# Optimization experiments

Hardware: AMD Instinct MI355X
Metric: run time of the kernel (lower is better)

The kernel has to match this reference:

```python
import jax, jax.numpy as jnp
import numpy as np

B, T, DIM, N_EMBED = 16, 2048, 512, 4096


def setup_inputs() -> dict:
    key = jax.random.key(0)
    k1, k2 = jax.random.split(key)
    x = jax.random.normal(k1, (B, T, DIM), dtype=jnp.float32)
    embed_weight = jax.random.normal(k2, (N_EMBED, DIM), dtype=jnp.float32)
    return {"x": x, "embed_weight": embed_weight}


def reference(x, embed_weight):
    dim = embed_weight.shape[1]
    # embed = embedding.weight.detach().T, column-normalized -> [dim, n_embed]
    w = jax.lax.stop_gradient(embed_weight).T
    w = w / jnp.linalg.norm(w, axis=0, keepdims=True)
    flatten = jax.lax.stop_gradient(x).reshape(-1, dim)  # [N, dim]
    # squared-distance expansion: |f|^2 - 2 f.w + |w|^2 -> [N, n_embed]
    dist = (
        jnp.sum(flatten * flatten, axis=1, keepdims=True)
        - 2.0 * (flatten @ w)
        + jnp.sum(w * w, axis=0, keepdims=True)
    )
    embed_ind = jnp.argmax(-dist, axis=1).reshape(x.shape[:-1])  # [B, T]
    # gather from the UN-normalized embedding table (as in the torch code)
    quantize = embed_weight[embed_ind]  # [B, T, dim]
    diff = jnp.mean(jnp.square(quantize - x))
    quantize_1 = x + jax.lax.stop_gradient(quantize - x)  # straight-through
    return ((quantize + quantize_1) * 0.5, diff)
```

## Files before the change

kernel.cpp:

```cpp
#include <hip/hip_runtime.h>
#include <math.h>

#define N_TOK   32768
#define N_CODE  4096
#define DIM     512

#define CBM 64
#define NHALF 2048
#define CBN 256
#define CBK 64
#define NT_STEPS (NHALF / CBN)
#define KC_STEPS (DIM / CBK)
#define SPITCH 36
#define BUFSZ 40960

#define SFENCE() __builtin_amdgcn_sched_barrier(0)

#define BARL() do { \
    SFENCE(); \
    asm volatile("s_waitcnt lgkmcnt(0)" ::: "memory"); \
    __builtin_amdgcn_s_barrier(); \
    SFENCE(); \
} while (0)

#define BAR_PUB10() do { \
    SFENCE(); \
    asm volatile("s_waitcnt vmcnt(10)" ::: "memory"); \
    __builtin_amdgcn_s_barrier(); \
    SFENCE(); \
} while (0)

#define BAR_PUB0() do { \
    SFENCE(); \
    asm volatile("s_waitcnt vmcnt(0)" ::: "memory"); \
    __builtin_amdgcn_s_barrier(); \
    SFENCE(); \
} while (0)

typedef __bf16 bf16x8 __attribute__((ext_vector_type(8)));
typedef float  f32x4  __attribute__((ext_vector_type(4)));

__device__ __forceinline__ unsigned short f32_to_bf16_rn(float f) {
    union { float f; unsigned int u; } c; c.f = f;
    unsigned int u = c.u;
    return (unsigned short)((u + 0x7FFFu + ((u >> 16) & 1u)) >> 16);
}

__device__ __forceinline__ unsigned f32_sortkey(float f) {
    unsigned u = __float_as_uint(f);
    return u ^ ((unsigned)(((int)u) >> 31) | 0x80000000u);
}

__device__ __forceinline__ void top8k_insert(unsigned s, unsigned (&bv)[8]) {
#pragma unroll
    for (int k = 7; k > 0; --k) {
        unsigned t = bv[k] > s ? bv[k] : s;
        bv[k] = (s > bv[k - 1]) ? bv[k - 1] : t;
    }
    bv[0] = bv[0] > s ? bv[0] : s;
}

__device__ __forceinline__ void top3k_insert(unsigned s, unsigned &b0,
                                             unsigned &b1, unsigned &b2) {
    unsigned t = b0 < s ? b0 : s;
    b0 = b0 > s ? b0 : s;
    unsigned u = b1 < t ? b1 : t;
    b1 = b1 > t ? b1 : t;
    b2 = b2 > u ? b2 : u;
}

__device__ __forceinline__ float pairwise_tree(const float* p) {
    float P[4];
#pragma unroll
    for (int b = 0; b < 4; ++b) {
        float t01 = __fadd_rn(p[b * 8 + 0], p[b * 8 + 1]);
        float t23 = __fadd_rn(p[b * 8 + 2], p[b * 8 + 3]);
        float t45 = __fadd_rn(p[b * 8 + 4], p[b * 8 + 5]);
        float t67 = __fadd_rn(p[b * 8 + 6], p[b * 8 + 7]);
        P[b] = __fadd_rn(__fadd_rn(t01, t23), __fadd_rn(t45, t67));
    }
    return __fadd_rn(__fadd_rn(P[0], P[1]), __fadd_rn(P[2], P[3]));
}

__global__ void norms_kernel(const float* __restrict__ embed,
                             float* __restrict__ n_f,
                             float* __restrict__ t3_f) {
    __shared__ float part[32];
    int j = blockIdx.x;
    int lane = threadIdx.x;
    const float* e = embed + (size_t)j * DIM;

    if (lane < 32) {
        int base = (lane >> 3) * 128 + (lane & 7);
        float v = e[base];
        float r = __fmul_rn(v, v);
#pragma unroll
        for (int i = 1; i < 16; ++i) {
            float u = e[base + 8 * i];
            r = __fadd_rn(r, __fmul_rn(u, u));
        }
        part[lane] = r;
    }
    __syncthreads();
    float S = pairwise_tree(part);
    float n = __fsqrt_rn(S);
    __syncthreads();

    if (lane < 32) {
        int base = (lane >> 3) * 128 + (lane & 7);
        float w0 = __fdiv_rn(e[base], n);
        float r = __fmul_rn(w0, w0);
#pragma unroll
        for (int i = 1; i < 16; ++i) {
            float w = __fdiv_rn(e[base + 8 * i], n);
            r = __fadd_rn(r, __fmul_rn(w, w));
        }
        part[lane] = r;
    }
    __syncthreads();
    if (lane == 0) {
        n_f[j]  = n;
        t3_f[j] = pairwise_tree(part);
    }
}

__global__ void xcvt_kernel(const float* __restrict__ x, unsigned short* __restrict__ xb) {
    int gid = blockIdx.x * 256 + threadIdx.x;
    float4 v = ((const float4*)x)[gid];
    ushort4 o;
    o.x = f32_to_bf16_rn(v.x); o.y = f32_to_bf16_rn(v.y);
    o.z = f32_to_bf16_rn(v.z); o.w = f32_to_bf16_rn(v.w);
    ((ushort4*)xb)[gid] = o;
}

__global__ void wcvt_kernel(const float* __restrict__ embed, const float* __restrict__ n_f,
                            float* __restrict__ whf, unsigned short* __restrict__ wb) {
    int gid = blockIdx.x * 256 + threadIdx.x;
    int row = gid >> 7;
    float n = n_f[row];
    float4 e = ((const float4*)embed)[gid];
    float4 w;
    w.x = __fdiv_rn(e.x, n); w.y = __fdiv_rn(e.y, n);
    w.z = __fdiv_rn(e.z, n); w.w = __fdiv_rn(e.w, n);
    ((float4*)whf)[gid] = w;
    ushort4 o;
    o.x = f32_to_bf16_rn(w.x); o.y = f32_to_bf16_rn(w.y);
    o.z = f32_to_bf16_rn(w.z); o.w = f32_to_bf16_rn(w.w);
    ((ushort4*)wb)[gid] = o;
}

__global__ __launch_bounds__(256, 2) void coarse_kernel(
        const unsigned short* __restrict__ xb,
        const unsigned short* __restrict__ wb,
        unsigned* __restrict__ candp) {
    __shared__ __attribute__((aligned(16))) char smem[2 * BUFSZ];

    const int tid  = threadIdx.x;
    const int w    = tid >> 6;
    const int l    = tid & 63;
    const int m0   = (blockIdx.x >> 1) * CBM;
    const int half = blockIdx.x & 1;
    const int n0   = half * NHALF;

    const int srow   = l >> 3;
    const int schunk = (l & 7) ^ srow;
    const int mrow   = l & 15;
    const int kq     = l >> 4;
    const int sw     = mrow & 7;

    const int aoff0 = mrow * 128 + (kq        ^ sw) * 16;
    const int aoff1 = mrow * 128 + ((kq ^ 4)  ^ sw) * 16;
    const int boff0 = 8192 + w * 8192 + mrow * 128 + (kq       ^ sw) * 16;
    const int boff1 = 8192 + w * 8192 + mrow * 128 + ((kq ^ 4) ^ sw) * 16;

    const unsigned short* gA0 = xb + (size_t)(m0 + w * 16 +     srow) * DIM + schunk * 8;
    const unsigned short* gA1 = xb + (size_t)(m0 + w * 16 + 8 + srow) * DIM + schunk * 8;
    const unsigned short* gB[8];
#pragma unroll
    for (int c = 0; c < 8; ++c)
        gB[c] = wb + (size_t)(n0 + w * 64 + c * 8 + srow) * DIM + schunk * 8;

    const int dA = w * 2048;
    const int dB = 8192 + w * 8192;

    auto STAGE = [&](int dstbuf, int koff) {
        char* db = smem + dstbuf * BUFSZ;
        __builtin_amdgcn_global_load_lds(
            (const __attribute__((address_space(1))) void*)(gA0 + koff),
            (__attribute__((address_space(3))) void*)(db + dA), 16, 0, 0);
        __builtin_amdgcn_global_load_lds(
            (const __attribute__((address_space(1))) void*)(gA1 + koff),
            (__attribute__((address_space(3))) void*)(db + dA + 1024), 16, 0, 0);
#pragma unroll
        for (int c = 0; c < 8; ++c)
            __builtin_amdgcn_global_load_lds(
                (const __attribute__((address_space(1))) void*)(gB[c] + koff),
                (__attribute__((address_space(3))) void*)(db + dB + c * 1024), 16, 0, 0);
    };

    unsigned* const sS  = (unsigned*)(smem + BUFSZ);
    unsigned* const swp = sS + w * (64 * SPITCH) + kq * (4 * SPITCH) + mrow;
    const uint4* const srp = (const uint4*)(sS + (tid >> 6) * (64 * SPITCH) + (tid & 63) * SPITCH);

    const int invb = 4095 - n0 - w * 64 - mrow;

    unsigned b0 = 0u, b1 = 0u, b2 = 0u;

    STAGE(0, 0);

    for (int nt = 0; nt < NT_STEPS; ++nt) {
        f32x4 acc[4][4];
#pragma unroll
        for (int i = 0; i < 4; ++i)
#pragma unroll
            for (int j = 0; j < 4; ++j) acc[i][j] = {0.0f, 0.0f, 0.0f, 0.0f};

#pragma unroll
        for (int kc = 0; kc < KC_STEPS; ++kc) {
            if (kc > 0) BARL();

            if (kc < KC_STEPS - 1) {
                STAGE((kc + 1) & 1, (kc + 1) * CBK);
                BAR_PUB10();
            } else if (nt < NT_STEPS - 1) {
#pragma unroll
                for (int c = 0; c < 8; ++c) gB[c] += (size_t)CBN * DIM;
                STAGE(0, 0);
                BAR_PUB10();
            } else {
                BAR_PUB0();
            }

            const int bb = (kc & 1) * BUFSZ;
            bf16x8 a0[4], bb0[4], a1[4], bb1[4];
#pragma unroll
            for (int i = 0; i < 4; ++i)
                a0[i] = *(const bf16x8*)(smem + bb + aoff0 + i * 2048);
#pragma unroll
            for (int j = 0; j < 4; ++j)
                bb0[j] = *(const bf16x8*)(smem + bb + boff0 + j * 2048);
#pragma unroll
            for (int i = 0; i < 4; ++i)
#pragma unroll
                for (int j = 0; j < 4; ++j)
                    acc[i][j] = __builtin_amdgcn_mfma_f32_16x16x32_bf16(
                        a0[i], bb0[j], acc[i][j], 0, 0, 0);
#pragma unroll
            for (int i = 0; i < 4; ++i)
                a1[i] = *(const bf16x8*)(smem + bb + aoff1 + i * 2048);
#pragma unroll
            for (int j = 0; j < 4; ++j)
                bb1[j] = *(const bf16x8*)(smem + bb + boff1 + j * 2048);
#pragma unroll
            for (int i = 0; i < 4; ++i)
#pragma unroll
                for (int j = 0; j < 4; ++j)
                    acc[i][j] = __builtin_amdgcn_mfma_f32_16x16x32_bf16(
                        a1[i], bb1[j], acc[i][j], 0, 0, 0);
        }

        BARL();
#pragma unroll
        for (int h = 0; h < 2; ++h) {
#pragma unroll
            for (int i = 0; i < 4; ++i)
#pragma unroll
                for (int jj = 0; jj < 2; ++jj) {
                    const int j = h * 2 + jj;
                    const unsigned ifld = (unsigned)(invb - (nt * 256 + h * 32 + jj * 16));
#pragma unroll
                    for (int r = 0; r < 4; ++r) {
                        unsigned key = (f32_sortkey(acc[i][j][r]) & 0xFFFFF000u) | ifld;
                        swp[(i * 16 + r) * SPITCH + jj * 16] = key;
                    }
                }
            BARL();
#pragma unroll
            for (int c4 = 0; c4 < 8; ++c4) {
                uint4 v = srp[c4];
                top3k_insert(v.x, b0, b1, b2);
                top3k_insert(v.y, b0, b1, b2);
                top3k_insert(v.z, b0, b1, b2);
                top3k_insert(v.w, b0, b1, b2);
            }
            BARL();
        }
    }

    {
        int tok = tid & 63, qq = tid >> 6;
        unsigned* cp = candp + ((size_t)(m0 + tok) * 2 + half) * 12 + qq * 3;
        cp[0] = b0; cp[1] = b1; cp[2] = b2;
    }
}

__global__ void merge_kernel(const unsigned* __restrict__ candp, int* __restrict__ cand8) {
    int tok = blockIdx.x * 256 + threadIdx.x;
    unsigned bv[8];
#pragma unroll
    for (int k = 0; k < 8; ++k) bv[k] = 0u;
    const unsigned* cp = candp + (size_t)tok * 24;
#pragma unroll
    for (int t = 0; t < 24; ++t) top8k_insert(cp[t], bv);
    int* o = cand8 + (size_t)tok * 8;
#pragma unroll
    for (int k = 0; k < 8; ++k) o[k] = 4095 - (int)(bv[k] & 0xFFFu);
}

__global__ void refine_kernel(const float* __restrict__ x,
                              const float* __restrict__ embed,
                              const float* __restrict__ whf,
                              const float* __restrict__ t3_f,
                              const int* __restrict__ cand,
                              float* __restrict__ out,
                              double* __restrict__ partial) {
    __shared__ float part[4][32];
    __shared__ double wsum[4];
    const int wid  = threadIdx.x >> 6;
    const int lane = threadIdx.x & 63;
    const int tok  = blockIdx.x * 4 + wid;
    const float* f = x + (size_t)tok * DIM;

    if (lane < 32) {
        int base = (lane >> 3) * 128 + (lane & 7);
        float v = f[base];
        float r = __fmul_rn(v, v);
#pragma unroll
        for (int i = 1; i < 16; ++i) {
            float u = f[base + 8 * i];
            r = __fadd_rn(r, __fmul_rn(u, u));
        }
        part[wid][lane] = r;
    }
    __syncthreads();
    float t1 = pairwise_tree(part[wid]);

    float4 f0 = *(const float4*)(f + lane * 8);
    float4 f1 = *(const float4*)(f + lane * 8 + 4);

    float bd = 1e30f; int bc = 0x7fffffff;
    const int* cp = cand + (size_t)tok * 8;
#pragma unroll
    for (int k = 0; k < 8; ++k) {
        int c = cp[k];
        const float* wh = whf + (size_t)c * DIM + lane * 8;
        float4 w0 = *(const float4*)wh;
        float4 w1 = *(const float4*)(wh + 4);
        double s = (double)f0.x * w0.x + (double)f0.y * w0.y
                 + (double)f0.z * w0.z + (double)f0.w * w0.w
                 + (double)f1.x * w1.x + (double)f1.y * w1.y
                 + (double)f1.z * w1.z + (double)f1.w * w1.w;
#pragma unroll
        for (int off = 32; off > 0; off >>= 1) s += __shfl_xor(s, off);
        float mm = (float)s;
        float dist = __fadd_rn(__fsub_rn(t1, __fmul_rn(2.0f, mm)), t3_f[c]);
        if (dist < bd || (dist == bd && c < bc)) { bd = dist; bc = c; }
    }

    const float* eb = embed + (size_t)bc * DIM;
    double dsum = 0.0;
#pragma unroll
    for (int r = 0; r < DIM / 64; ++r) {
        int d = lane + 64 * r;
        float q = eb[d];
        out[(size_t)tok * DIM + d] = q;
        double dd = (double)q - (double)f[d];
        dsum += dd * dd;
    }
#pragma unroll
    for (int off = 32; off > 0; off >>= 1) dsum += __shfl_xor(dsum, off);
    if (lane == 0) wsum[wid] = dsum;
    __syncthreads();
    if (threadIdx.x == 0)
        partial[blockIdx.x] = wsum[0] + wsum[1] + wsum[2] + wsum[3];
}

__global__ void finalize_kernel(const double* __restrict__ partial,
                                float* __restrict__ out) {
    __shared__ double acc[4];
    int tid = threadIdx.x;
    double s = 0.0;
    for (int i = tid; i < N_TOK / 4; i += 256) s += partial[i];
#pragma unroll
    for (int off = 32; off > 0; off >>= 1) s += __shfl_xor(s, off);
    if ((tid & 63) == 0) acc[tid >> 6] = s;
    __syncthreads();
    if (tid == 0)
        out[(size_t)N_TOK * DIM] =
            (float)((acc[0] + acc[1] + acc[2] + acc[3]) * (1.0 / ((double)N_TOK * DIM)));
}

extern "C" void kernel_launch(void* const* d_in, const int* in_sizes, int n_in,
                              void* d_out, int out_size, void* d_ws, size_t ws_size,
                              hipStream_t stream) {
    const float* x     = (const float*)d_in[0];
    const float* embed = (const float*)d_in[1];
    float* out = (float*)d_out;

    char* wsb = (char*)d_ws;
    size_t off = 0;
    double* partial = (double*)(wsb + off); off += 65536;
    float*  n_f     = (float*) (wsb + off); off += 16384;
    float*  t3_f    = (float*) (wsb + off); off += 16384;
    unsigned* candp = (unsigned*)(wsb + off); off += (size_t)N_TOK * 24 * 4;
    int*    cand8   = (int*)   (wsb + off); off += (size_t)N_TOK * 8 * 4;
    unsigned short* xb = (unsigned short*)(wsb + off); off += (size_t)N_TOK * DIM * 2;
    unsigned short* wb = (unsigned short*)(wsb + off); off += (size_t)N_CODE * DIM * 2;
    float*  whf     = (float*) (wsb + off);

    xcvt_kernel    <<<16384, 256, 0, stream>>>(x, xb);
    norms_kernel   <<<N_CODE, 64, 0, stream>>>(embed, n_f, t3_f);
    wcvt_kernel    <<<2048, 256, 0, stream>>>(embed, n_f, whf, wb);
    coarse_kernel  <<<(N_TOK / CBM) * 2, 256, 0, stream>>>(xb, wb, candp);
    merge_kernel   <<<N_TOK / 256, 256, 0, stream>>>(candp, cand8);
    refine_kernel  <<<N_TOK / 4, 256, 0, stream>>>(x, embed, whf, t3_f, cand8, out, partial);
    finalize_kernel<<<1, 256, 0, stream>>>(partial, out);
}
```

Baseline: 373.5 us.

## Keep per-token top-3 candidates in registers and reduce in-block before writing

Swaps the MFMA operand order so each lane's accumulator rows map to a single token. The per-tile LDS transpose plus its two barriers go away, and top-3 tracking runs directly in registers with one list per accumulator row. At the end, the 16 per-lane top-3 lists for each token are merged through LDS into a top-8, which shrinks the candidate buffer and the merge work. The register pressure of 12 extra keys and the more serial insert chain per lane may affect occupancy. Candidate recall also changes, since each token's list now comes from per-lane top-3 over a different column split.

```diff
diff --git a/kernel.cpp b/kernel.cpp
--- a/kernel.cpp
+++ b/kernel.cpp
@@ -11,7 +11,6 @@
 #define CBK 64
 #define NT_STEPS (NHALF / CBN)
 #define KC_STEPS (DIM / CBK)
-#define SPITCH 36
 #define BUFSZ 40960
 
 #define SFENCE() __builtin_amdgcn_sched_barrier(0)
@@ -198,13 +197,9 @@
                 (__attribute__((address_space(3))) void*)(db + dB + c * 1024), 16, 0, 0);
     };
 
-    unsigned* const sS  = (unsigned*)(smem + BUFSZ);
-    unsigned* const swp = sS + w * (64 * SPITCH) + kq * (4 * SPITCH) + mrow;
-    const uint4* const srp = (const uint4*)(sS + (tid >> 6) * (64 * SPITCH) + (tid & 63) * SPITCH);
-
-    const int invb = 4095 - n0 - w * 64 - mrow;
-
-    unsigned b0 = 0u, b1 = 0u, b2 = 0u;
+    unsigned k0[4], k1[4], k2[4];
+#pragma unroll
+    for (int i = 0; i < 4; ++i) { k0[i] = 0u; k1[i] = 0u; k2[i] = 0u; }
 
     STAGE(0, 0);
 
@@ -217,7 +212,8 @@
 
 #pragma unroll
         for (int kc = 0; kc < KC_STEPS; ++kc) {
-            if (kc > 0) BARL();
+            if (kc > 0) { BARL(); }
+            else if (nt > 0) { BARL(); }
 
             if (kc < KC_STEPS - 1) {
                 STAGE((kc + 1) & 1, (kc + 1) * CBK);
@@ -244,7 +240,7 @@
 #pragma unroll
                 for (int j = 0; j < 4; ++j)
                     acc[i][j] = __builtin_amdgcn_mfma_f32_16x16x32_bf16(
-                        a0[i], bb0[j], acc[i][j], 0, 0, 0);
+                        bb0[j], a0[i], acc[i][j], 0, 0, 0);
 #pragma unroll
             for (int i = 0; i < 4; ++i)
                 a1[i] = *(const bf16x8*)(smem + bb + aoff1 + i * 2048);
@@ -256,41 +252,50 @@
 #pragma unroll
                 for (int j = 0; j < 4; ++j)
                     acc[i][j] = __builtin_amdgcn_mfma_f32_16x16x32_bf16(
-                        a1[i], bb1[j], acc[i][j], 0, 0, 0);
-        }
-
-        BARL();
-#pragma unroll
-        for (int h = 0; h < 2; ++h) {
+                        bb1[j], a1[i], acc[i][j], 0, 0, 0);
+        }
+
+        {
+            const unsigned inb = (unsigned)(4095 - n0 - w * 64 - kq * 4 - nt * 256);
 #pragma unroll
             for (int i = 0; i < 4; ++i)
 #pragma unroll
-                for (int jj = 0; jj < 2; ++jj) {
-                    const int j = h * 2 + jj;
-                    const unsigned ifld = (unsigned)(invb - (nt * 256 + h * 32 + jj * 16));
+                for (int j = 0; j < 4; ++j)
 #pragma unroll
                     for (int r = 0; r < 4; ++r) {
-                        unsigned key = (f32_sortkey(acc[i][j][r]) & 0xFFFFF000u) | ifld;
-                        swp[(i * 16 + r) * SPITCH + jj * 16] = key;
+                        unsigned key = (f32_sortkey(acc[i][j][r]) & 0xFFFFF000u)
+                                     | (inb - (unsigned)(j * 16 + r));
+                        top3k_insert(key, k0[i], k1[i], k2[i]);
                     }
-                }
-            BARL();
-#pragma unroll
-            for (int c4 = 0; c4 < 8; ++c4) {
-                uint4 v = srp[c4];
-                top3k_insert(v.x, b0, b1, b2);
-                top3k_insert(v.y, b0, b1, b2);
-                top3k_insert(v.z, b0, b1, b2);
-                top3k_insert(v.w, b0, b1, b2);
-            }
-            BARL();
         }
     }
 
     {
-        int tok = tid & 63, qq = tid >> 6;
-        unsigned* cp = candp + ((size_t)(m0 + tok) * 2 + half) * 12 + qq * 3;
-        cp[0] = b0; cp[1] = b1; cp[2] = b2;
+        unsigned* ck = (unsigned*)smem;
+        const int slot = w * 4 + kq;
+#pragma unroll
+        for (int i = 0; i < 4; ++i) {
+            unsigned* p = ck + ((size_t)(i * 16 + mrow) * 16 + slot) * 3;
+            p[0] = k0[i]; p[1] = k1[i]; p[2] = k2[i];
+        }
+    }
+    BARL();
+    if (tid < 64) {
+        const uint4* cq = (const uint4*)smem + tid * 12;
+        unsigned fv[8];
+#pragma unroll
+        for (int k = 0; k < 8; ++k) fv[k] = 0u;
+#pragma unroll
+        for (int t = 0; t < 12; ++t) {
+            uint4 v = cq[t];
+            top8k_insert(v.x, fv);
+            top8k_insert(v.y, fv);
+            top8k_insert(v.z, fv);
+            top8k_insert(v.w, fv);
+        }
+        unsigned* cp = candp + ((size_t)(m0 + tid) * 2 + half) * 8;
+#pragma unroll
+        for (int k = 0; k < 8; ++k) cp[k] = fv[k];
     }
 }
 
@@ -299,9 +304,9 @@
     unsigned bv[8];
 #pragma unroll
     for (int k = 0; k < 8; ++k) bv[k] = 0u;
-    const unsigned* cp = candp + (size_t)tok * 24;
-#pragma unroll
-    for (int t = 0; t < 24; ++t) top8k_insert(cp[t], bv);
+    const unsigned* cp = candp + (size_t)tok * 16;
+#pragma unroll
+    for (int t = 0; t < 16; ++t) top8k_insert(cp[t], bv);
     int* o = cand8 + (size_t)tok * 8;
 #pragma unroll
     for (int k = 0; k < 8; ++k) o[k] = 4095 - (int)(bv[k] & 0xFFFu);
@@ -402,7 +407,7 @@
     double* partial = (double*)(wsb + off); off += 65536;
     float*  n_f     = (float*) (wsb + off); off += 16384;
     float*  t3_f    = (float*) (wsb + off); off += 16384;
-    unsigned* candp = (unsigned*)(wsb + off); off += (size_t)N_TOK * 24 * 4;
+    unsigned* candp = (unsigned*)(wsb + off); off += (size_t)N_TOK * 16 * 4;
     int*    cand8   = (int*)   (wsb + off); off += (size_t)N_TOK * 8 * 4;
     unsigned short* xb = (unsigned short*)(wsb + off); off += (size_t)N_TOK * DIM * 2;
     unsigned short* wb = (unsigned short*)(wsb + off); off += (size_t)N_CODE * DIM * 2;
```

Measured after the change: 368.9 us. Within noise of the previous version (-1.2%).
